# Kernel optimization log

Measured on AMD Instinct MI355X. Metric: run time of the kernel, lower is better.

## Reference

```python
import jax, jax.numpy as jnp
import numpy as np

B, T, H, N_CMD, N_OUT = 2048, 128, 512, 3, 5
IN_DIM = N_OUT + N_CMD  # 8


def setup_inputs() -> dict:
    key = jax.random.key(0)
    ks = jax.random.split(key, 16)
    s = 0.1
    return {
        'predict_len': T,
        'rnn_input_commands': jax.random.normal(ks[0], (T, B, N_CMD), jnp.float32),
        'y0': jax.random.normal(ks[1], (B, N_OUT), jnp.float32),
        'h0_1': jax.random.normal(ks[2], (B, H), jnp.float32),
        'h0_2': jax.random.normal(ks[3], (B, H), jnp.float32),
        # GRUCell layer 1 (input dim 8)
        'W_ih1': jax.random.normal(ks[4], (3 * H, IN_DIM), jnp.float32) * s,
        'W_hh1': jax.random.normal(ks[5], (3 * H, H), jnp.float32) * s,
        'b_ih1': jax.random.normal(ks[6], (3 * H,), jnp.float32) * s,
        'b_hh1': jax.random.normal(ks[7], (3 * H,), jnp.float32) * s,
        # GRUCell layer 2 (input dim H)
        'W_ih2': jax.random.normal(ks[8], (3 * H, H), jnp.float32) * s,
        'W_hh2': jax.random.normal(ks[9], (3 * H, H), jnp.float32) * s,
        'b_ih2': jax.random.normal(ks[10], (3 * H,), jnp.float32) * s,
        'b_hh2': jax.random.normal(ks[11], (3 * H,), jnp.float32) * s,
        # linear head
        'W_out': jax.random.normal(ks[12], (N_OUT, H), jnp.float32) * s,
        'b_out': jax.random.normal(ks[13], (N_OUT,), jnp.float32) * s,
    }


def _gru_cell(x, h, W_ih, W_hh, b_ih, b_hh):
    # PyTorch GRUCell: gates ordered (r, z, n)
    gi = x @ W_ih.T + b_ih  # [B, 3H]
    gh = h @ W_hh.T + b_hh  # [B, 3H]
    i_r, i_z, i_n = jnp.split(gi, 3, axis=-1)
    h_r, h_z, h_n = jnp.split(gh, 3, axis=-1)
    r = jax.nn.sigmoid(i_r + h_r)
    z = jax.nn.sigmoid(i_z + h_z)
    n = jnp.tanh(i_n + r * h_n)
    return (1.0 - z) * n + z * h


def reference(predict_len, rnn_input_commands, y0, h0_1, h0_2,
              W_ih1, W_hh1, b_ih1, b_hh1,
              W_ih2, W_hh2, b_ih2, b_hh2,
              W_out, b_out):
    cmds = rnn_input_commands[:predict_len]  # [T, B, n_cmd]

    def step(carry, cmd_t):
        y, h1, h2 = carry
        x = jnp.concatenate([y, cmd_t], axis=1)  # [B, n_out + n_cmd]
        h1 = _gru_cell(x, h1, W_ih1, W_hh1, b_ih1, b_hh1)
        h2 = _gru_cell(h1, h2, W_ih2, W_hh2, b_ih2, b_hh2)
        y = h2 @ W_out.T + b_out  # [B, n_out]
        return (y, h1, h2), y

    _, ys = jax.lax.scan(step, (y0, h0_1, h0_2), cmds)
    # torch.stack(self.outputs, 1) -> [B, T, n_out]
    return jnp.transpose(ys, (1, 0, 2))
```

## Files before the change

### kernel.cpp

```cpp
#include <hip/hip_runtime.h>
#include <math.h>

#define B 2048
#define T 128
#define H 512
#define NC 3
#define NO 5
#define G3H 1536
#define BHE ((size_t)B * H)

typedef _Float16 half8 __attribute__((ext_vector_type(8)));
typedef float float4v __attribute__((ext_vector_type(4)));

#define LO_SCALE 1024.0f
#define INV_LO (1.0f / 1024.0f)
#define F16_MIN_NORM 6.103515625e-05f

__device__ __forceinline__ float sigmoidf_(float x) { return 1.0f / (1.0f + __expf(-x)); }

__device__ __forceinline__ void split_f16(float a, _Float16* hi, _Float16* lo) {
    _Float16 h = (_Float16)a;
    if (fabsf(a) < F16_MIN_NORM) h = (_Float16)0.0f;
    *hi = h;
    *lo = (_Float16)((a - (float)h) * LO_SCALE);
}

__device__ __forceinline__ int swzk(int row, int k) {
    return (k & ~63) | ((((k >> 3) & 7) ^ (row & 7)) << 3) | (k & 7);
}
__device__ __forceinline__ size_t hidx(int row, int k) {
    return (size_t)row * H + swzk(row, k);
}

__device__ __forceinline__ void stage16(const _Float16* gp, _Float16* lp) {
    __builtin_amdgcn_global_load_lds(
        (const __attribute__((address_space(1))) unsigned int*)gp,
        (__attribute__((address_space(3))) unsigned int*)lp,
        16, 0, 0);
}

__global__ void conv3_kernel(const float* __restrict__ w1, const float* __restrict__ w2,
                             const float* __restrict__ w3,
                             _Float16* o1h, _Float16* o1l, _Float16* o2h, _Float16* o2l,
                             _Float16* o3h, _Float16* o3l) {
    int i = blockIdx.x * 256 + threadIdx.x;
    if (i < G3H * H) {
        const int r = i >> 9, k = i & 511;
        const size_t d = (size_t)r * H + swzk(r, k);
        split_f16(w1[i], &o1h[d], &o1l[d]);
        split_f16(w2[i], &o2h[d], &o2l[d]);
        split_f16(w3[i], &o3h[d], &o3l[d]);
    }
}

__global__ void prep_kernel(const float* __restrict__ h01, const float* __restrict__ h02,
                            _Float16* h1h, _Float16* h1l, _Float16* h2h, _Float16* h2l) {
    int i = blockIdx.x * 256 + threadIdx.x;
    if (i < B * H) {
        const int r = i >> 9, k = i & 511;
        const size_t d = (size_t)r * H + swzk(r, k);
        split_f16(h01[i], &h1h[d], &h1l[d]);
        split_f16(h02[i], &h2h[d], &h2l[d]);
    }
}

__device__ __forceinline__ void stage_tile32(
    const _Float16* __restrict__ Ahp, const _Float16* __restrict__ Alp,
    const _Float16* __restrict__ Whp, const _Float16* __restrict__ Wlp,
    int m0, int n0, int k0, int tid, int wv,
    _Float16* sAh, _Float16* sAl, _Float16* sWh, _Float16* sWl)
{
    {
        const int row = tid >> 3, kc = tid & 7;
        const size_t off = (size_t)(m0 + row) * H + k0 + kc * 8;
        stage16(Ahp + off, &sAh[(wv * 64) * 8]);
        stage16(Alp + off, &sAl[(wv * 64) * 8]);
    }
    {
        const int g = tid >> 8, rem = tid & 255;
        const int nr = rem >> 3, kc = rem & 7;
        const size_t off = (size_t)(g * H + n0 + nr) * H + k0 + kc * 8;
        stage16(Whp + off, &sWh[(wv * 64) * 8]);
        stage16(Wlp + off, &sWl[(wv * 64) * 8]);
    }
    if (tid < 256) {
        const int nr = tid >> 3, kc = tid & 7;
        const size_t off = (size_t)(2 * H + n0 + nr) * H + k0 + kc * 8;
        stage16(Whp + off, &sWh[(512 + wv * 64) * 8]);
        stage16(Wlp + off, &sWl[(512 + wv * 64) * 8]);
    }
}

template <int SN, int NS>
__device__ __forceinline__ void compute_tile32(
    const _Float16* sAh_, const _Float16* sAl_,
    const _Float16* sWh_, const _Float16* sWl_,
    int wm, int wn, int ln, int qd,
    float4v (&accH)[NS], float4v (&accL)[NS])
{
    #pragma unroll
    for (int ks = 0; ks < 2; ++ks) {
        const int c = ks * 4 + qd;
        const int row = wm * 16 + ln;
        const int ai = row * 64 + ((c ^ (row & 7)) << 3);
        half8 afh = *(const half8*)&sAh_[ai];
        half8 afl = *(const half8*)&sAl_[ai];
        const int nr = wn * 16 + ln;
        #pragma unroll
        for (int g = 0; g < 3; ++g) {
            const int s = (g < 2) ? g : SN;
            const int wi = (g * 32 + nr) * 64 + ((c ^ (nr & 7)) << 3);
            half8 bh = *(const half8*)&sWh_[wi];
            half8 bl = *(const half8*)&sWl_[wi];
            accH[s] = __builtin_amdgcn_mfma_f32_16x16x32_f16(afh, bh, accH[s], 0, 0, 0);
            accL[s] = __builtin_amdgcn_mfma_f32_16x16x32_f16(afh, bl, accL[s], 0, 0, 0);
            accL[s] = __builtin_amdgcn_mfma_f32_16x16x32_f16(afl, bh, accL[s], 0, 0, 0);
        }
    }
}

__global__ __launch_bounds__(512, 4) void gru1_kernel(
    const _Float16* __restrict__ Ah, const _Float16* __restrict__ Al,
    const _Float16* __restrict__ Wh, const _Float16* __restrict__ Wl,
    const float* __restrict__ ypart,
    const float* __restrict__ bout,
    const float* __restrict__ y0, const float* __restrict__ cmd_t,
    const float* __restrict__ W_ih1,
    const float* __restrict__ b_ih1, const float* __restrict__ b_hh1,
    _Float16* __restrict__ hnh, _Float16* __restrict__ hnl,
    float* __restrict__ out, int t)
{
    __shared__ _Float16 sAh[2][4096], sAl[2][4096];
    __shared__ _Float16 sWh[2][6144], sWl[2][6144];

    const int tid = threadIdx.x;
    const int wv = tid >> 6, lane = tid & 63;
    const int wm = wv >> 1, wn = wv & 1;
    const int ln = lane & 15, qd = lane >> 4;
    const int n0 = (blockIdx.x & 15) * 32;
    const int m0 = (blockIdx.x >> 4) * 64;

    stage_tile32(Ah, Al, Wh, Wl, m0, n0, 0, tid, wv, sAh[0], sAl[0], sWh[0], sWl[0]);

    float4v accH[3], accL[3];
    #pragma unroll
    for (int s = 0; s < 3; ++s) { accH[s] = (float4v)(0.f); accL[s] = (float4v)(0.f); }

    for (int it = 0; it < 8; ++it) {
        const int buf = it & 1;
        __syncthreads();
        if (it + 1 < 8)
            stage_tile32(Ah, Al, Wh, Wl, m0, n0, (it + 1) * 64, tid, wv,
                         sAh[buf ^ 1], sAl[buf ^ 1], sWh[buf ^ 1], sWl[buf ^ 1]);
        compute_tile32<2, 3>(sAh[buf], sAl[buf], sWh[buf], sWl[buf], wm, wn, ln, qd, accH, accL);
    }

    float* sX = (float*)&sAh[0][0];
    const int yr = tid >> 3, yp = tid & 7;
    if (t == 0) {
        if (tid < 64) {
            #pragma unroll
            for (int o2 = 0; o2 < NO; ++o2)
                sX[tid * 8 + o2] = y0[(size_t)(m0 + tid) * NO + o2];
        }
    } else {
        const int row = m0 + yr;
        float a5[NO];
        #pragma unroll
        for (int o2 = 0; o2 < NO; ++o2) {
            const float4 v = *(const float4*)(ypart + ((size_t)row * NO + o2) * 32 + yp * 4);
            a5[o2] = (v.x + v.y) + (v.z + v.w);
        }
        #pragma unroll
        for (int off = 1; off < 8; off <<= 1)
            #pragma unroll
            for (int o2 = 0; o2 < NO; ++o2) a5[o2] += __shfl_xor(a5[o2], off, 64);
        if (yp == 0) {
            #pragma unroll
            for (int o2 = 0; o2 < NO; ++o2) {
                const float y = a5[o2] + bout[o2];
                sX[yr * 8 + o2] = y;
                if (n0 == 0)
                    out[(size_t)(m0 + yr) * (T * NO) + (size_t)(t - 1) * NO + o2] = y;
            }
        }
    }
    if (tid < 64) {
        #pragma unroll
        for (int c = 0; c < NC; ++c)
            sX[tid * 8 + NO + c] = cmd_t[(size_t)(m0 + tid) * NC + c];
    }
    __syncthreads();

    const int gnl = wn * 16 + ln;
    const int gn = n0 + gnl;
    float wi[3][8];
    #pragma unroll
    for (int g = 0; g < 3; ++g) {
        const float4 w0 = *(const float4*)(W_ih1 + (size_t)(g * H + gn) * 8);
        const float4 w1 = *(const float4*)(W_ih1 + (size_t)(g * H + gn) * 8 + 4);
        wi[g][0] = w0.x; wi[g][1] = w0.y; wi[g][2] = w0.z; wi[g][3] = w0.w;
        wi[g][4] = w1.x; wi[g][5] = w1.y; wi[g][6] = w1.z; wi[g][7] = w1.w;
    }
    const float bi0 = b_ih1[0 * H + gn], bi1 = b_ih1[1 * H + gn], bi2 = b_ih1[2 * H + gn];
    const float bh0 = b_hh1[0 * H + gn], bh1 = b_hh1[1 * H + gn], bh2 = b_hh1[2 * H + gn];
    #pragma unroll
    for (int r = 0; r < 4; ++r) {
        const int mloc = wm * 16 + qd * 4 + r;
        const int m = m0 + mloc;
        float giR = bi0, giZ = bi1, giN = bi2;
        #pragma unroll
        for (int k = 0; k < 8; ++k) {
            const float xv = sX[mloc * 8 + k];
            giR = fmaf(xv, wi[0][k], giR);
            giZ = fmaf(xv, wi[1][k], giZ);
            giN = fmaf(xv, wi[2][k], giN);
        }
        const float gR = giR + bh0 + accH[0][r] + accL[0][r] * INV_LO;
        const float gZ = giZ + bh1 + accH[1][r] + accL[1][r] * INV_LO;
        const float gNh = bh2 + accH[2][r] + accL[2][r] * INV_LO;
        const float R = sigmoidf_(gR), Z = sigmoidf_(gZ);
        const float N = tanhf(fmaf(R, gNh, giN));
        const size_t idx = hidx(m, gn);
        const float hp = (float)Ah[idx] + (float)Al[idx] * INV_LO;
        const float hv = (1.f - Z) * N + Z * hp;
        split_f16(hv, &hnh[idx], &hnl[idx]);
    }
}

__global__ __launch_bounds__(512, 4) void gru2_kernel(
    const _Float16* __restrict__ Aih, const _Float16* __restrict__ Ail,
    const _Float16* __restrict__ Wih, const _Float16* __restrict__ Wil,
    const _Float16* __restrict__ Ahh, const _Float16* __restrict__ Ahl,
    const _Float16* __restrict__ Whh, const _Float16* __restrict__ Whl,
    const float* __restrict__ b_i, const float* __restrict__ b_h,
    const float* __restrict__ Wout,
    _Float16* __restrict__ hnh, _Float16* __restrict__ hnl,
    float* __restrict__ ypart)
{
    __shared__ _Float16 sAh[2][4096], sAl[2][4096];
    __shared__ _Float16 sWh[2][6144], sWl[2][6144];

    const int tid = threadIdx.x;
    const int wv = tid >> 6, lane = tid & 63;
    const int wm = wv >> 1, wn = wv & 1;
    const int ln = lane & 15, qd = lane >> 4;
    const int n0 = (blockIdx.x & 15) * 32;
    const int m0 = (blockIdx.x >> 4) * 64;

    float4v accH[4], accL[4];
    #pragma unroll
    for (int s = 0; s < 4; ++s) { accH[s] = (float4v)(0.f); accL[s] = (float4v)(0.f); }

    stage_tile32(Aih, Ail, Wih, Wil, m0, n0, 0, tid, wv, sAh[0], sAl[0], sWh[0], sWl[0]);
    for (int it = 0; it < 16; ++it) {
        const int buf = it & 1;
        __syncthreads();
        if (it + 1 < 16) {
            const int k0 = ((it + 1) & 7) * 64;
            if (it + 1 < 8)
                stage_tile32(Aih, Ail, Wih, Wil, m0, n0, k0, tid, wv,
                             sAh[buf ^ 1], sAl[buf ^ 1], sWh[buf ^ 1], sWl[buf ^ 1]);
            else
                stage_tile32(Ahh, Ahl, Whh, Whl, m0, n0, k0, tid, wv,
                             sAh[buf ^ 1], sAl[buf ^ 1], sWh[buf ^ 1], sWl[buf ^ 1]);
        }
        if (it < 8)
            compute_tile32<2, 4>(sAh[buf], sAl[buf], sWh[buf], sWl[buf], wm, wn, ln, qd, accH, accL);
        else
            compute_tile32<3, 4>(sAh[buf], sAl[buf], sWh[buf], sWl[buf], wm, wn, ln, qd, accH, accL);
    }

    const int gnl = wn * 16 + ln;
    const int gn = n0 + gnl;
    const float bi0 = b_i[0 * H + gn], bi1 = b_i[1 * H + gn], bi2 = b_i[2 * H + gn];
    const float bh0 = b_h[0 * H + gn], bh1 = b_h[1 * H + gn], bh2 = b_h[2 * H + gn];
    const float wo0 = Wout[0 * H + gn], wo1 = Wout[1 * H + gn], wo2 = Wout[2 * H + gn];
    const float wo3 = Wout[3 * H + gn], wo4 = Wout[4 * H + gn];
    const int ws = (blockIdx.x & 15) * 2 + wn;
    #pragma unroll
    for (int r = 0; r < 4; ++r) {
        const int m = m0 + wm * 16 + qd * 4 + r;
        const float gR = bi0 + bh0 + accH[0][r] + accL[0][r] * INV_LO;
        const float gZ = bi1 + bh1 + accH[1][r] + accL[1][r] * INV_LO;
        const float gNi = bi2 + accH[2][r] + accL[2][r] * INV_LO;
        const float gNh = bh2 + accH[3][r] + accL[3][r] * INV_LO;
        const float R = sigmoidf_(gR), Z = sigmoidf_(gZ);
        const float N = tanhf(fmaf(R, gNh, gNi));
        const size_t idx = hidx(m, gn);
        const float hp = (float)Ahh[idx] + (float)Ahl[idx] * INV_LO;
        const float hv = (1.f - Z) * N + Z * hp;
        split_f16(hv, &hnh[idx], &hnl[idx]);

        float p0 = hv * wo0, p1 = hv * wo1, p2 = hv * wo2, p3 = hv * wo3, p4 = hv * wo4;
        #pragma unroll
        for (int off = 1; off < 16; off <<= 1) {
            p0 += __shfl_xor(p0, off, 64);
            p1 += __shfl_xor(p1, off, 64);
            p2 += __shfl_xor(p2, off, 64);
            p3 += __shfl_xor(p3, off, 64);
            p4 += __shfl_xor(p4, off, 64);
        }
        if (ln == 0) {
            float* yp = ypart + (size_t)m * NO * 32 + ws;
            yp[0 * 32] = p0;
            yp[1 * 32] = p1;
            yp[2 * 32] = p2;
            yp[3 * 32] = p3;
            yp[4 * 32] = p4;
        }
    }
}

__global__ __launch_bounds__(256) void yout_final_kernel(
    const _Float16* __restrict__ h2h, const _Float16* __restrict__ h2l,
    const float* __restrict__ Wout, const float* __restrict__ bout,
    float* __restrict__ out)
{
    const int wv = threadIdx.x >> 6, lane = threadIdx.x & 63;
    const int b = blockIdx.x * 4 + wv;
    const size_t hb = (size_t)b * H + lane * 8;
    half8 hh = *(const half8*)(h2h + hb);
    half8 hl = *(const half8*)(h2l + hb);
    const int tl = lane >> 3, cw = lane & 7;
    const int kbase = tl * 64 + ((cw ^ (b & 7)) << 3);
    float hv[8];
    #pragma unroll
    for (int j = 0; j < 8; ++j) hv[j] = (float)hh[j] + (float)hl[j] * INV_LO;
    float acc[NO];
    #pragma unroll
    for (int o = 0; o < NO; ++o) {
        acc[o] = 0.f;
        const float* w = Wout + (size_t)o * H + kbase;
        #pragma unroll
        for (int j = 0; j < 8; ++j) acc[o] = fmaf(hv[j], w[j], acc[o]);
    }
    #pragma unroll
    for (int off = 32; off > 0; off >>= 1)
        #pragma unroll
        for (int o = 0; o < NO; ++o) acc[o] += __shfl_down(acc[o], off, 64);
    if (lane == 0) {
        #pragma unroll
        for (int o = 0; o < NO; ++o)
            out[(size_t)b * (T * NO) + (size_t)(T - 1) * NO + o] = acc[o] + bout[o];
    }
}

extern "C" void kernel_launch(void* const* d_in, const int* in_sizes, int n_in,
                              void* d_out, int out_size, void* d_ws, size_t ws_size,
                              hipStream_t stream) {
    (void)in_sizes; (void)n_in; (void)out_size; (void)ws_size;
    const float* cmds  = (const float*)d_in[1];
    const float* y0    = (const float*)d_in[2];
    const float* h01   = (const float*)d_in[3];
    const float* h02   = (const float*)d_in[4];
    const float* W_ih1 = (const float*)d_in[5];
    const float* W_hh1 = (const float*)d_in[6];
    const float* b_ih1 = (const float*)d_in[7];
    const float* b_hh1 = (const float*)d_in[8];
    const float* W_ih2 = (const float*)d_in[9];
    const float* W_hh2 = (const float*)d_in[10];
    const float* b_ih2 = (const float*)d_in[11];
    const float* b_hh2 = (const float*)d_in[12];
    const float* W_out = (const float*)d_in[13];
    const float* b_out = (const float*)d_in[14];
    float* out = (float*)d_out;

    char* ws = (char*)d_ws;
    size_t o = 0;
    const size_t WSZ = (size_t)G3H * H * sizeof(_Float16);
    _Float16* wh1h = (_Float16*)(ws + o); o += WSZ;
    _Float16* wh1l = (_Float16*)(ws + o); o += WSZ;
    _Float16* wi2h = (_Float16*)(ws + o); o += WSZ;
    _Float16* wi2l = (_Float16*)(ws + o); o += WSZ;
    _Float16* wh2h = (_Float16*)(ws + o); o += WSZ;
    _Float16* wh2l = (_Float16*)(ws + o); o += WSZ;
    _Float16 *h1h[2], *h1l[2], *h2h[2], *h2l[2];
    for (int i = 0; i < 2; ++i) { h1h[i] = (_Float16*)(ws + o); o += BHE * 2; }
    for (int i = 0; i < 2; ++i) { h1l[i] = (_Float16*)(ws + o); o += BHE * 2; }
    for (int i = 0; i < 2; ++i) { h2h[i] = (_Float16*)(ws + o); o += BHE * 2; }
    for (int i = 0; i < 2; ++i) { h2l[i] = (_Float16*)(ws + o); o += BHE * 2; }
    float* ypart = (float*)(ws + o); o += (size_t)B * NO * 32 * sizeof(float);

    conv3_kernel<<<(G3H * H + 255) / 256, 256, 0, stream>>>(
        W_hh1, W_ih2, W_hh2, wh1h, wh1l, wi2h, wi2l, wh2h, wh2l);
    prep_kernel<<<(B * H + 255) / 256, 256, 0, stream>>>(
        h01, h02, h1h[0], h1l[0], h2h[0], h2l[0]);

    for (int t = 0; t < T; ++t) {
        const int si = t & 1, so = si ^ 1;

        gru1_kernel<<<512, 512, 0, stream>>>(
            h1h[si], h1l[si], wh1h, wh1l,
            ypart, b_out,
            y0, cmds + (size_t)t * B * NC,
            W_ih1, b_ih1, b_hh1,
            h1h[so], h1l[so],
            out, t);

        gru2_kernel<<<512, 512, 0, stream>>>(
            h1h[so], h1l[so], wi2h, wi2l,
            h2h[si], h2l[si], wh2h, wh2l,
            b_ih2, b_hh2, W_out,
            h2h[so], h2l[so],
            ypart);
    }

    yout_final_kernel<<<B / 4, 256, 0, stream>>>(
        h2h[0], h2l[0], W_out, b_out, out);
}
```

Before: 5.910 ms.

## Split K across wave pairs with 32x16 warp tiles and LDS reduction

Changes the warp decomposition in both GRU kernels. Each wave now computes a 32-row by 16-column tile (two M sub-tiles that share each B fragment) over half of every 64-wide K chunk, instead of a 16x16 tile over the full chunk. The two K-halves are summed through shared memory after the main loop. This raises B-fragment reuse per LDS read and halves the MFMA chain per wave. The cost is twice the accumulator registers, an extra LDS reduction with another barrier, and half the waves sitting idle during the epilogue.

Measured after the change: 6.508 ms. +10.1%, slower.

```diff
diff --git a/kernel.cpp b/kernel.cpp
--- a/kernel.cpp
+++ b/kernel.cpp
@@ -38,6 +38,11 @@
         (__attribute__((address_space(3))) unsigned int*)lp,
         16, 0, 0);
 }
+
+#define SAH(b) (smem + (b) * 4096)
+#define SAL(b) (smem + 8192 + (b) * 4096)
+#define SWH(b) (smem + 16384 + (b) * 6144)
+#define SWL(b) (smem + 28672 + (b) * 6144)
 
 __global__ void conv3_kernel(const float* __restrict__ w1, const float* __restrict__ w2,
                              const float* __restrict__ w3,
@@ -92,29 +97,33 @@
 }
 
 template <int SN, int NS>
-__device__ __forceinline__ void compute_tile32(
+__device__ __forceinline__ void compute_half(
     const _Float16* sAh_, const _Float16* sAl_,
     const _Float16* sWh_, const _Float16* sWl_,
-    int wm, int wn, int ln, int qd,
-    float4v (&accH)[NS], float4v (&accL)[NS])
+    int wm, int wn, int kh, int ln, int qd,
+    float4v (&accH)[NS][2], float4v (&accL)[NS][2])
 {
-    #pragma unroll
-    for (int ks = 0; ks < 2; ++ks) {
-        const int c = ks * 4 + qd;
-        const int row = wm * 16 + ln;
+    const int c = kh * 4 + qd;
+    half8 afh[2], afl[2];
+    #pragma unroll
+    for (int ms = 0; ms < 2; ++ms) {
+        const int row = wm * 32 + ms * 16 + ln;
         const int ai = row * 64 + ((c ^ (row & 7)) << 3);
-        half8 afh = *(const half8*)&sAh_[ai];
-        half8 afl = *(const half8*)&sAl_[ai];
-        const int nr = wn * 16 + ln;
-        #pragma unroll
-        for (int g = 0; g < 3; ++g) {
-            const int s = (g < 2) ? g : SN;
-            const int wi = (g * 32 + nr) * 64 + ((c ^ (nr & 7)) << 3);
-            half8 bh = *(const half8*)&sWh_[wi];
-            half8 bl = *(const half8*)&sWl_[wi];
-            accH[s] = __builtin_amdgcn_mfma_f32_16x16x32_f16(afh, bh, accH[s], 0, 0, 0);
-            accL[s] = __builtin_amdgcn_mfma_f32_16x16x32_f16(afh, bl, accL[s], 0, 0, 0);
-            accL[s] = __builtin_amdgcn_mfma_f32_16x16x32_f16(afl, bh, accL[s], 0, 0, 0);
+        afh[ms] = *(const half8*)&sAh_[ai];
+        afl[ms] = *(const half8*)&sAl_[ai];
+    }
+    const int nr = wn * 16 + ln;
+    #pragma unroll
+    for (int g = 0; g < 3; ++g) {
+        const int s = (g < 2) ? g : SN;
+        const int wi = (g * 32 + nr) * 64 + ((c ^ (nr & 7)) << 3);
+        half8 bh = *(const half8*)&sWh_[wi];
+        half8 bl = *(const half8*)&sWl_[wi];
+        #pragma unroll
+        for (int ms = 0; ms < 2; ++ms) {
+            accH[s][ms] = __builtin_amdgcn_mfma_f32_16x16x32_f16(afh[ms], bh, accH[s][ms], 0, 0, 0);
+            accL[s][ms] = __builtin_amdgcn_mfma_f32_16x16x32_f16(afh[ms], bl, accL[s][ms], 0, 0, 0);
+            accL[s][ms] = __builtin_amdgcn_mfma_f32_16x16x32_f16(afl[ms], bh, accL[s][ms], 0, 0, 0);
         }
     }
 }
@@ -130,32 +139,47 @@
     _Float16* __restrict__ hnh, _Float16* __restrict__ hnl,
     float* __restrict__ out, int t)
 {
-    __shared__ _Float16 sAh[2][4096], sAl[2][4096];
-    __shared__ _Float16 sWh[2][6144], sWl[2][6144];
+    __shared__ _Float16 smem[40960];
 
     const int tid = threadIdx.x;
     const int wv = tid >> 6, lane = tid & 63;
-    const int wm = wv >> 1, wn = wv & 1;
+    const int kh = wv & 1, wn = (wv >> 1) & 1, wm = wv >> 2;
     const int ln = lane & 15, qd = lane >> 4;
     const int n0 = (blockIdx.x & 15) * 32;
     const int m0 = (blockIdx.x >> 4) * 64;
 
-    stage_tile32(Ah, Al, Wh, Wl, m0, n0, 0, tid, wv, sAh[0], sAl[0], sWh[0], sWl[0]);
-
-    float4v accH[3], accL[3];
-    #pragma unroll
-    for (int s = 0; s < 3; ++s) { accH[s] = (float4v)(0.f); accL[s] = (float4v)(0.f); }
+    stage_tile32(Ah, Al, Wh, Wl, m0, n0, 0, tid, wv, SAH(0), SAL(0), SWH(0), SWL(0));
+
+    float4v accH[3][2], accL[3][2];
+    #pragma unroll
+    for (int s = 0; s < 3; ++s)
+        #pragma unroll
+        for (int ms = 0; ms < 2; ++ms) { accH[s][ms] = (float4v)(0.f); accL[s][ms] = (float4v)(0.f); }
 
     for (int it = 0; it < 8; ++it) {
         const int buf = it & 1;
         __syncthreads();
         if (it + 1 < 8)
             stage_tile32(Ah, Al, Wh, Wl, m0, n0, (it + 1) * 64, tid, wv,
-                         sAh[buf ^ 1], sAl[buf ^ 1], sWh[buf ^ 1], sWl[buf ^ 1]);
-        compute_tile32<2, 3>(sAh[buf], sAl[buf], sWh[buf], sWl[buf], wm, wn, ln, qd, accH, accL);
-    }
-
-    float* sX = (float*)&sAh[0][0];
+                         SAH(buf ^ 1), SAL(buf ^ 1), SWH(buf ^ 1), SWL(buf ^ 1));
+        compute_half<2, 3>(SAH(buf), SAL(buf), SWH(buf), SWL(buf), wm, wn, kh, ln, qd, accH, accL);
+    }
+
+    __syncthreads();
+
+    float4v* mg = (float4v*)(smem + 16384);
+    const int pr = wm * 2 + wn;
+    if (kh == 1) {
+        #pragma unroll
+        for (int s = 0; s < 3; ++s)
+            #pragma unroll
+            for (int ms = 0; ms < 2; ++ms) {
+                mg[(s * 2 + ms) * 256 + pr * 64 + lane] = accH[s][ms];
+                mg[(6 + s * 2 + ms) * 256 + pr * 64 + lane] = accL[s][ms];
+            }
+    }
+
+    float* sX = (float*)&smem[0];
     const int yr = tid >> 3, yp = tid & 7;
     if (t == 0) {
         if (tid < 64) {
@@ -192,6 +216,16 @@
     }
     __syncthreads();
 
+    if (kh != 0) return;
+
+    #pragma unroll
+    for (int s = 0; s < 3; ++s)
+        #pragma unroll
+        for (int ms = 0; ms < 2; ++ms) {
+            accH[s][ms] += mg[(s * 2 + ms) * 256 + pr * 64 + lane];
+            accL[s][ms] += mg[(6 + s * 2 + ms) * 256 + pr * 64 + lane];
+        }
+
     const int gnl = wn * 16 + ln;
     const int gn = n0 + gnl;
     float wi[3][8];
@@ -205,26 +239,29 @@
     const float bi0 = b_ih1[0 * H + gn], bi1 = b_ih1[1 * H + gn], bi2 = b_ih1[2 * H + gn];
     const float bh0 = b_hh1[0 * H + gn], bh1 = b_hh1[1 * H + gn], bh2 = b_hh1[2 * H + gn];
     #pragma unroll
-    for (int r = 0; r < 4; ++r) {
-        const int mloc = wm * 16 + qd * 4 + r;
-        const int m = m0 + mloc;
-        float giR = bi0, giZ = bi1, giN = bi2;
-        #pragma unroll
-        for (int k = 0; k < 8; ++k) {
-            const float xv = sX[mloc * 8 + k];
-            giR = fmaf(xv, wi[0][k], giR);
-            giZ = fmaf(xv, wi[1][k], giZ);
-            giN = fmaf(xv, wi[2][k], giN);
-        }
-        const float gR = giR + bh0 + accH[0][r] + accL[0][r] * INV_LO;
-        const float gZ = giZ + bh1 + accH[1][r] + accL[1][r] * INV_LO;
-        const float gNh = bh2 + accH[2][r] + accL[2][r] * INV_LO;
-        const float R = sigmoidf_(gR), Z = sigmoidf_(gZ);
-        const float N = tanhf(fmaf(R, gNh, giN));
-        const size_t idx = hidx(m, gn);
-        const float hp = (float)Ah[idx] + (float)Al[idx] * INV_LO;
-        const float hv = (1.f - Z) * N + Z * hp;
-        split_f16(hv, &hnh[idx], &hnl[idx]);
+    for (int ms = 0; ms < 2; ++ms) {
+        #pragma unroll
+        for (int r = 0; r < 4; ++r) {
+            const int mloc = wm * 32 + ms * 16 + qd * 4 + r;
+            const int m = m0 + mloc;
+            float giR = bi0, giZ = bi1, giN = bi2;
+            #pragma unroll
+            for (int k = 0; k < 8; ++k) {
+                const float xv = sX[mloc * 8 + k];
+                giR = fmaf(xv, wi[0][k], giR);
+                giZ = fmaf(xv, wi[1][k], giZ);
+                giN = fmaf(xv, wi[2][k], giN);
+            }
+            const float gR = giR + bh0 + accH[0][ms][r] + accL[0][ms][r] * INV_LO;
+            const float gZ = giZ + bh1 + accH[1][ms][r] + accL[1][ms][r] * INV_LO;
+            const float gNh = bh2 + accH[2][ms][r] + accL[2][ms][r] * INV_LO;
+            const float R = sigmoidf_(gR), Z = sigmoidf_(gZ);
+            const float N = tanhf(fmaf(R, gNh, giN));
+            const size_t idx = hidx(m, gn);
+            const float hp = (float)Ah[idx] + (float)Al[idx] * INV_LO;
+            const float hv = (1.f - Z) * N + Z * hp;
+            split_f16(hv, &hnh[idx], &hnl[idx]);
+        }
     }
 }
 
@@ -238,21 +275,22 @@
     _Float16* __restrict__ hnh, _Float16* __restrict__ hnl,
     float* __restrict__ ypart)
 {
-    __shared__ _Float16 sAh[2][4096], sAl[2][4096];
-    __shared__ _Float16 sWh[2][6144], sWl[2][6144];
+    __shared__ _Float16 smem[40960];
 
     const int tid = threadIdx.x;
     const int wv = tid >> 6, lane = tid & 63;
-    const int wm = wv >> 1, wn = wv & 1;
+    const int kh = wv & 1, wn = (wv >> 1) & 1, wm = wv >> 2;
     const int ln = lane & 15, qd = lane >> 4;
     const int n0 = (blockIdx.x & 15) * 32;
     const int m0 = (blockIdx.x >> 4) * 64;
 
-    float4v accH[4], accL[4];
-    #pragma unroll
-    for (int s = 0; s < 4; ++s) { accH[s] = (float4v)(0.f); accL[s] = (float4v)(0.f); }
-
-    stage_tile32(Aih, Ail, Wih, Wil, m0, n0, 0, tid, wv, sAh[0], sAl[0], sWh[0], sWl[0]);
+    float4v accH[4][2], accL[4][2];
+    #pragma unroll
+    for (int s = 0; s < 4; ++s)
+        #pragma unroll
+        for (int ms = 0; ms < 2; ++ms) { accH[s][ms] = (float4v)(0.f); accL[s][ms] = (float4v)(0.f); }
+
+    stage_tile32(Aih, Ail, Wih, Wil, m0, n0, 0, tid, wv, SAH(0), SAL(0), SWH(0), SWL(0));
     for (int it = 0; it < 16; ++it) {
         const int buf = it & 1;
         __syncthreads();
@@ -260,16 +298,40 @@
             const int k0 = ((it + 1) & 7) * 64;
             if (it + 1 < 8)
                 stage_tile32(Aih, Ail, Wih, Wil, m0, n0, k0, tid, wv,
-                             sAh[buf ^ 1], sAl[buf ^ 1], sWh[buf ^ 1], sWl[buf ^ 1]);
+                             SAH(buf ^ 1), SAL(buf ^ 1), SWH(buf ^ 1), SWL(buf ^ 1));
             else
                 stage_tile32(Ahh, Ahl, Whh, Whl, m0, n0, k0, tid, wv,
-                             sAh[buf ^ 1], sAl[buf ^ 1], sWh[buf ^ 1], sWl[buf ^ 1]);
+                             SAH(buf ^ 1), SAL(buf ^ 1), SWH(buf ^ 1), SWL(buf ^ 1));
         }
         if (it < 8)
-            compute_tile32<2, 4>(sAh[buf], sAl[buf], sWh[buf], sWl[buf], wm, wn, ln, qd, accH, accL);
+            compute_half<2, 4>(SAH(buf), SAL(buf), SWH(buf), SWL(buf), wm, wn, kh, ln, qd, accH, accL);
         else
-            compute_tile32<3, 4>(sAh[buf], sAl[buf], sWh[buf], sWl[buf], wm, wn, ln, qd, accH, accL);
-    }
+            compute_half<3, 4>(SAH(buf), SAL(buf), SWH(buf), SWL(buf), wm, wn, kh, ln, qd, accH, accL);
+    }
+
+    __syncthreads();
+
+    float4v* mg = (float4v*)smem;
+    const int pr = wm * 2 + wn;
+    if (kh == 1) {
+        #pragma unroll
+        for (int s = 0; s < 4; ++s)
+            #pragma unroll
+            for (int ms = 0; ms < 2; ++ms) {
+                mg[(s * 2 + ms) * 256 + pr * 64 + lane] = accH[s][ms];
+                mg[(8 + s * 2 + ms) * 256 + pr * 64 + lane] = accL[s][ms];
+            }
+    }
+    __syncthreads();
+    if (kh != 0) return;
+
+    #pragma unroll
+    for (int s = 0; s < 4; ++s)
+        #pragma unroll
+        for (int ms = 0; ms < 2; ++ms) {
+            accH[s][ms] += mg[(s * 2 + ms) * 256 + pr * 64 + lane];
+            accL[s][ms] += mg[(8 + s * 2 + ms) * 256 + pr * 64 + lane];
+        }
 
     const int gnl = wn * 16 + ln;
     const int gn = n0 + gnl;
@@ -279,35 +341,38 @@
     const float wo3 = Wout[3 * H + gn], wo4 = Wout[4 * H + gn];
     const int ws = (blockIdx.x & 15) * 2 + wn;
     #pragma unroll
-    for (int r = 0; r < 4; ++r) {
-        const int m = m0 + wm * 16 + qd * 4 + r;
-        const float gR = bi0 + bh0 + accH[0][r] + accL[0][r] * INV_LO;
-        const float gZ = bi1 + bh1 + accH[1][r] + accL[1][r] * INV_LO;
-        const float gNi = bi2 + accH[2][r] + accL[2][r] * INV_LO;
-        const float gNh = bh2 + accH[3][r] + accL[3][r] * INV_LO;
-        const float R = sigmoidf_(gR), Z = sigmoidf_(gZ);
-        const float N = tanhf(fmaf(R, gNh, gNi));
-        const size_t idx = hidx(m, gn);
-        const float hp = (float)Ahh[idx] + (float)Ahl[idx] * INV_LO;
-        const float hv = (1.f - Z) * N + Z * hp;
-        split_f16(hv, &hnh[idx], &hnl[idx]);
-
-        float p0 = hv * wo0, p1 = hv * wo1, p2 = hv * wo2, p3 = hv * wo3, p4 = hv * wo4;
-        #pragma unroll
-        for (int off = 1; off < 16; off <<= 1) {
-            p0 += __shfl_xor(p0, off, 64);
-            p1 += __shfl_xor(p1, off, 64);
-            p2 += __shfl_xor(p2, off, 64);
-            p3 += __shfl_xor(p3, off, 64);
-            p4 += __shfl_xor(p4, off, 64);
-        }
-        if (ln == 0) {
-            float* yp = ypart + (size_t)m * NO * 32 + ws;
-            yp[0 * 32] = p0;
-            yp[1 * 32] = p1;
-            yp[2 * 32] = p2;
-            yp[3 * 32] = p3;
-            yp[4 * 32] = p4;
+    for (int ms = 0; ms < 2; ++ms) {
+        #pragma unroll
+        for (int r = 0; r < 4; ++r) {
+            const int m = m0 + wm * 32 + ms * 16 + qd * 4 + r;
+            const float gR = bi0 + bh0 + accH[0][ms][r] + accL[0][ms][r] * INV_LO;
+            const float gZ = bi1 + bh1 + accH[1][ms][r] + accL[1][ms][r] * INV_LO;
+            const float gNi = bi2 + accH[2][ms][r] + accL[2][ms][r] * INV_LO;
+            const float gNh = bh2 + accH[3][ms][r] + accL[3][ms][r] * INV_LO;
+            const float R = sigmoidf_(gR), Z = sigmoidf_(gZ);
+            const float N = tanhf(fmaf(R, gNh, gNi));
+            const size_t idx = hidx(m, gn);
+            const float hp = (float)Ahh[idx] + (float)Ahl[idx] * INV_LO;
+            const float hv = (1.f - Z) * N + Z * hp;
+            split_f16(hv, &hnh[idx], &hnl[idx]);
+
+            float p0 = hv * wo0, p1 = hv * wo1, p2 = hv * wo2, p3 = hv * wo3, p4 = hv * wo4;
+            #pragma unroll
+            for (int off = 1; off < 16; off <<= 1) {
+                p0 += __shfl_xor(p0, off, 64);
+                p1 += __shfl_xor(p1, off, 64);
+                p2 += __shfl_xor(p2, off, 64);
+                p3 += __shfl_xor(p3, off, 64);
+                p4 += __shfl_xor(p4, off, 64);
+            }
+            if (ln == 0) {
+                float* yp = ypart + (size_t)m * NO * 32 + ws;
+                yp[0 * 32] = p0;
+                yp[1 * 32] = p1;
+                yp[2 * 32] = p2;
+                yp[3 * 32] = p3;
+                yp[4 * 32] = p4;
+            }
         }
     }
 }
```
